# Performance work log

Measured on AMD Instinct MI355X. Metric: run time of the kernel, lower is better.

The kernel has to match this reference:

```python
import jax, jax.numpy as jnp
import numpy as np

B, S, D = 4, 2048, 768
H = 12
DH = D // H
NUM_WAY = 4
DFF = 4 * D  # FFN expansion scale=4
EPS = 1e-6


def setup_inputs() -> dict:
    key = jax.random.key(0)
    ks = jax.random.split(key, 20)
    s = 0.02
    inp = {
        "x": jax.random.normal(ks[0], (B, S, D), jnp.float32),
        "w": jax.random.randint(ks[1], (B, S), 0, NUM_WAY, jnp.int64),
        # LayerNorm 1
        "ln1_g": jnp.ones((D,), jnp.float32),
        "ln1_b": jnp.zeros((D,), jnp.float32),
        # Multi-head attention projections (input_dim=out_dim=D)
        "wq": jax.random.normal(ks[2], (D, D), jnp.float32) * s,
        "bq": jnp.zeros((D,), jnp.float32),
        "wk": jax.random.normal(ks[3], (D, D), jnp.float32) * s,
        "bk": jnp.zeros((D,), jnp.float32),
        "wv": jax.random.normal(ks[4], (D, D), jnp.float32) * s,
        "bv": jnp.zeros((D,), jnp.float32),
        "wo": jax.random.normal(ks[5], (D, D), jnp.float32) * s,
        "bo": jnp.zeros((D,), jnp.float32),
        # Way classifier
        "wcls": jax.random.normal(ks[6], (D, NUM_WAY), jnp.float32) * s,
        "bcls": jnp.zeros((NUM_WAY,), jnp.float32),
        # num_way stacked FFN experts: Linear(D,4D) -> ReLU -> Linear(4D,D)
        "w1": jax.random.normal(ks[7], (NUM_WAY, D, DFF), jnp.float32) * s,
        "b1": jnp.zeros((NUM_WAY, DFF), jnp.float32),
        "w2": jax.random.normal(ks[8], (NUM_WAY, DFF, D), jnp.float32) * s,
        "b2": jnp.zeros((NUM_WAY, D), jnp.float32),
    }
    return inp


def _layernorm(x, g, b):
    mu = jnp.mean(x, axis=-1, keepdims=True)
    var = jnp.mean(jnp.square(x - mu), axis=-1, keepdims=True)
    return (x - mu) * jax.lax.rsqrt(var + EPS) * g + b


def reference(x, w, ln1_g, ln1_b, wq, bq, wk, bk, wv, bv, wo, bo,
              wcls, bcls, w1, b1, w2, b2):
    # pre-LN
    xn = _layernorm(x, ln1_g, ln1_b)
    # multi-head self-attention (q = k = v = xn)
    q = (xn @ wq + bq).reshape(B, S, H, DH)
    k = (xn @ wk + bk).reshape(B, S, H, DH)
    v = (xn @ wv + bv).reshape(B, S, H, DH)
    scores = jnp.einsum('bqhd,bkhd->bhqk', q, k) / jnp.sqrt(jnp.float32(DH))
    attn = jax.nn.softmax(scores, axis=-1)
    ctx = jnp.einsum('bhqk,bkhd->bqhd', attn, v).reshape(B, S, D)
    ctx = ctx @ wo + bo
    # dropout is identity at inference; residual
    out = ctx + x
    # dense compute-all-experts FFN, then per-token select by routing id w
    # (mask-overwrite in original == one-hot select since masks partition)
    ffn_out = jnp.zeros_like(out)
    for ci in range(NUM_WAY):
        h = jax.nn.relu(out @ w1[ci] + b1[ci])        # [B,S,4D]
        fi = h @ w2[ci] + b2[ci]                      # [B,S,D]
        mask = (w == ci).astype(out.dtype)[..., None]  # [B,S,1]
        if ci == 0:
            # original initializes ffn_out with way-0 output everywhere;
            # later ways overwrite where w == ci, net = select expert w
            ffn_out = fi
        else:
            ffn_out = ffn_out * (1.0 - mask) + fi * mask
    way_logits = out @ wcls + bcls  # [B,S,NUM_WAY]
    return ffn_out, way_logits
```

## Files before the change

kernel.cpp:

```cpp
#include <hip/hip_runtime.h>
#include <cstdint>

typedef unsigned short u16;
typedef float f32x4 __attribute__((ext_vector_type(4)));
typedef float f32x16 __attribute__((ext_vector_type(16)));
typedef __bf16 bf16x8 __attribute__((ext_vector_type(8)));

#define LOG2E 1.44269504088896340736f

__device__ __forceinline__ u16 f2bf(float f) {
    union { float f; unsigned u; } v; v.f = f;
    unsigned r = v.u + 0x7fffu + ((v.u >> 16) & 1u);
    return (u16)(r >> 16);
}

__device__ __forceinline__ unsigned cvt_pk_bf16(float lo, float hi) {
    unsigned r;
    asm("v_cvt_pk_bf16_f32 %0, %1, %2" : "=v"(r) : "v"(lo), "v"(hi));
    return r;
}

__device__ __forceinline__ float exp2_hw(float x) {
    float r;
    asm("v_exp_f32 %0, %1" : "=v"(r) : "v"(x));
    return r;
}

__device__ __forceinline__ f32x4 mfma16(bf16x8 a, bf16x8 b, f32x4 c) {
    return __builtin_amdgcn_mfma_f32_16x16x32_bf16(a, b, c, 0, 0, 0);
}

__device__ __forceinline__ f32x16 mfma32(bf16x8 a, bf16x8 b, f32x16 c) {
    return __builtin_amdgcn_mfma_f32_32x32x16_bf16(a, b, c, 0, 0, 0);
}

__device__ __forceinline__ void gload_lds16(const void* g, void* l) {
    __builtin_amdgcn_global_load_lds(
        (__attribute__((address_space(1))) unsigned int*)(g),
        (__attribute__((address_space(3))) unsigned int*)(l),
        16, 0, 0);
}

#define MB_TOK 8192
#define DM 768
#define HH 12
#define DHD 64
#define NWAY 4
#define DFF 3072
#define SEQ 2048
#define NBATCH 4

__global__ __launch_bounds__(256) void ln_kernel(
    const float* __restrict__ x, const float* __restrict__ g,
    const float* __restrict__ bb, u16* __restrict__ xn)
{
    int row = blockIdx.x, t = threadIdx.x;
    const float* xr = x + (size_t)row * DM;
    float v0 = xr[t], v1 = xr[t + 256], v2 = xr[t + 512];
    float s = v0 + v1 + v2;
    __shared__ float red[4];
    #pragma unroll
    for (int k = 1; k < 64; k <<= 1) s += __shfl_xor(s, k);
    if ((t & 63) == 0) red[t >> 6] = s;
    __syncthreads();
    float mu = (red[0] + red[1] + red[2] + red[3]) * (1.f / 768.f);
    float d0 = v0 - mu, d1 = v1 - mu, d2 = v2 - mu;
    float q = d0 * d0 + d1 * d1 + d2 * d2;
    #pragma unroll
    for (int k = 1; k < 64; k <<= 1) q += __shfl_xor(q, k);
    __syncthreads();
    if ((t & 63) == 0) red[t >> 6] = q;
    __syncthreads();
    float var = (red[0] + red[1] + red[2] + red[3]) * (1.f / 768.f);
    float rs = rsqrtf(var + 1e-6f);
    u16* xo = xn + (size_t)row * DM;
    xo[t]       = f2bf(d0 * rs * g[t]       + bb[t]);
    xo[t + 256] = f2bf(d1 * rs * g[t + 256] + bb[t + 256]);
    xo[t + 512] = f2bf(d2 * rs * g[t + 512] + bb[t + 512]);
}

__global__ __launch_bounds__(256) void transpose_bf16(
    const float* __restrict__ src, u16* __restrict__ dst, int K, int N)
{
    __shared__ float tl[32][33];
    size_t bofs = (size_t)blockIdx.z * K * N;
    src += bofs; dst += bofs;
    int n0 = blockIdx.x * 32, k0 = blockIdx.y * 32;
    int tx = threadIdx.x, ty = threadIdx.y;
    #pragma unroll
    for (int j = 0; j < 4; ++j)
        tl[ty + j * 8][tx] = src[(size_t)(k0 + ty + j * 8) * N + n0 + tx];
    __syncthreads();
    #pragma unroll
    for (int j = 0; j < 4; ++j)
        dst[(size_t)(n0 + ty + j * 8) * K + k0 + tx] = f2bf(tl[tx][ty + j * 8]);
}

__global__ __launch_bounds__(256) void vT_kernel(
    const u16* __restrict__ qkv, u16* __restrict__ vT)
{
    __shared__ u16 tl[32][33];
    int bh = blockIdx.z;
    int b = bh / HH, h = bh % HH;
    int key0 = blockIdx.x * 32;
    int d0 = blockIdx.y * 32;
    int tx = threadIdx.x, ty = threadIdx.y;
    const u16* src = qkv + ((size_t)b * SEQ + key0) * 2304 + 1536 + h * 64 + d0;
    #pragma unroll
    for (int j = 0; j < 4; ++j)
        tl[ty + j * 8][tx] = src[(size_t)(ty + j * 8) * 2304 + tx];
    __syncthreads();
    u16* dst = vT + ((size_t)bh * 64 + d0) * SEQ + key0;
    #pragma unroll
    for (int j = 0; j < 4; ++j)
        dst[(size_t)(ty + j * 8) * SEQ + tx] = tl[tx][ty + j * 8];
}

__global__ void concat_bias_kernel(const float* bq, const float* bk,
                                   const float* bv, float* bqkv)
{
    int i = blockIdx.x * 256 + threadIdx.x;
    if (i < 2304) bqkv[i] = i < 768 ? bq[i] : (i < 1536 ? bk[i - 768] : bv[i - 1536]);
}

__global__ void route_kernel(const int* __restrict__ wl,
                             int* __restrict__ perm, int* __restrict__ eoff,
                             int4* __restrict__ fmap)
{
    __shared__ int cnt[4], cur[4], off[5];
    int tid = threadIdx.x;
    if (tid < 4) cnt[tid] = 0;
    __syncthreads();
    for (int t = tid; t < MB_TOK; t += 256) atomicAdd(&cnt[wl[t] & 3], 1);
    __syncthreads();
    if (tid == 0) {
        off[0] = 0;
        for (int e = 0; e < 4; ++e) off[e + 1] = off[e] + cnt[e];
        int idx = 0;
        for (int e = 0; e < 4; ++e)
            for (int s = 0; s < cnt[e]; s += 128)
                fmap[idx++] = make_int4(e, off[e], s, cnt[e] - s);
        for (; idx < 68; ++idx) fmap[idx] = make_int4(-1, 0, 0, 0);
        for (int e = 0; e < 5; ++e) eoff[e] = off[e];
        for (int e = 0; e < 4; ++e) cur[e] = off[e];
    }
    __syncthreads();
    for (int t = tid; t < MB_TOK; t += 256) {
        int e = wl[t] & 3;
        int pos = atomicAdd(&cur[e], 1);
        perm[pos] = t;
    }
}

template<int MODE, bool RELU, bool RES, bool ST32, bool ST16>
__global__ __launch_bounds__(256, 2) void gemm_bt_kernel(
    const u16* __restrict__ A, const u16* __restrict__ Bt,
    const float* __restrict__ bias, const float* __restrict__ res,
    float* __restrict__ out32, u16* __restrict__ out16,
    int M, int N, int K, int ntn,
    const int* __restrict__ perm, const int4* __restrict__ fmap)
{
    __shared__ __attribute__((aligned(16))) u16 As[128 * 32];
    __shared__ __attribute__((aligned(16))) u16 Bs[128 * 32];
    int tid = threadIdx.x;
    int wv = tid >> 6, ln = tid & 63;
    int bt = blockIdx.x / ntn;
    int tn = (blockIdx.x % ntn) * 128;

    int seg = 0, ms = 0, mb = 128, tm = 0;
    if (MODE != 0) {
        int4 ent = fmap[bt];
        if (ent.x < 0) return;
        seg = ent.y; ms = ent.z; mb = ent.w; if (mb > 128) mb = 128;
        Bt += (size_t)ent.x * N * K;
        bias += ent.x * N;
    } else {
        tm = bt * 128;
    }

    f32x4 acc[4][4];
    #pragma unroll
    for (int i = 0; i < 4; ++i)
        #pragma unroll
        for (int j = 0; j < 4; ++j) acc[i][j] = f32x4{0.f, 0.f, 0.f, 0.f};

    int wr = wv >> 1, wc = wv & 1;
    int lr = ln & 15, hi = ln >> 4;
    int nk = K / 32;

    for (int kk = 0; kk < nk; ++kk) {
        int k0 = kk * 32;
        #pragma unroll
        for (int i = 0; i < 2; ++i) {
            int r = (wv * 2 + i) * 16 + (ln >> 2);
            int am = r < mb ? r : (mb - 1);
            size_t arow;
            if (MODE == 1)      arow = (size_t)perm[seg + ms + am];
            else if (MODE == 2) arow = (size_t)(seg + ms + am);
            else                arow = (size_t)(tm + r);
            gload_lds16(A + arow * K + k0 + (ln & 3) * 8, &As[(wv * 2 + i) * 512]);
        }
        #pragma unroll
        for (int i = 0; i < 2; ++i) {
            int r = (wv * 2 + i) * 16 + (ln >> 2);
            gload_lds16(Bt + (size_t)(tn + r) * K + k0 + (ln & 3) * 8,
                        &Bs[(wv * 2 + i) * 512]);
        }
        __syncthreads();
        bf16x8 a[4], b[4];
        #pragma unroll
        for (int m = 0; m < 4; ++m)
            a[m] = *(const bf16x8*)&As[(wr * 64 + m * 16 + lr) * 32 + hi * 8];
        #pragma unroll
        for (int n = 0; n < 4; ++n)
            b[n] = *(const bf16x8*)&Bs[(wc * 64 + n * 16 + lr) * 32 + hi * 8];
        #pragma unroll
        for (int m = 0; m < 4; ++m)
            #pragma unroll
            for (int n = 0; n < 4; ++n)
                acc[m][n] = mfma16(a[m], b[n], acc[m][n]);
        __syncthreads();
    }

    #pragma unroll
    for (int m = 0; m < 4; ++m) {
        int rb = wr * 64 + m * 16 + hi * 4;
        #pragma unroll
        for (int n = 0; n < 4; ++n) {
            int gcol = tn + wc * 64 + n * 16 + lr;
            float bvv = bias[gcol];
            #pragma unroll
            for (int i = 0; i < 4; ++i) {
                int rml = rb + i;
                float v = acc[m][n][i] + bvv;
                if (RELU) v = v > 0.f ? v : 0.f;
                if (MODE == 0) {
                    size_t grow = (size_t)(tm + rml);
                    if (RES) v += res[grow * N + gcol];
                    if (ST32) out32[grow * N + gcol] = v;
                    if (ST16) out16[grow * N + gcol] = f2bf(v);
                } else {
                    if (rml < mb) {
                        size_t orow = (MODE == 1) ? (size_t)(seg + ms + rml)
                                                  : (size_t)perm[seg + ms + rml];
                        if (ST32) out32[orow * N + gcol] = v;
                        if (ST16) out16[orow * N + gcol] = f2bf(v);
                    }
                }
            }
        }
    }
}

__global__ __launch_bounds__(256, 4) void attn_kernel(
    const u16* __restrict__ qkv, const u16* __restrict__ vT,
    u16* __restrict__ ctx)
{
    __shared__ __attribute__((aligned(16))) u16 Ks[2][4096];
    __shared__ __attribute__((aligned(16))) u16 Vs[2][4096];
    int tid = threadIdx.x;
    int wv = tid >> 6, ln = tid & 63;
    int qv = ln & 31, hi = ln >> 5;
    int bid = blockIdx.x;
    int bh = (bid & 7) * 6 + ((bid >> 3) % 6);
    int qt = (bid >> 3) / 6;
    int b = bh / HH, h = bh % HH;
    int q0 = qt * 128 + wv * 32;
    size_t qrowb = (size_t)(b * SEQ + q0);
    const float C = 0.125f * LOG2E;

    bf16x8 qf[4];
    {
        const u16* qp = qkv + (qrowb + qv) * 2304 + h * 64 + hi * 8;
        #pragma unroll
        for (int ds = 0; ds < 4; ++ds) qf[ds] = *(const bf16x8*)(qp + ds * 16);
    }

    int csrc = 8 * ((ln & 7) ^ (ln >> 3));
    const size_t kbase = (size_t)b * SEQ * 2304 + 768 + h * 64;
    const u16* vtb = vT + (size_t)bh * 64 * SEQ;
    const u16* kp0 = qkv + kbase + (size_t)(wv * 16 + (ln >> 3)) * 2304 + csrc;
    const u16* kp1 = kp0 + (size_t)8 * 2304;
    const u16* vp0 = vtb + (size_t)(wv * 16 + (ln >> 3)) * SEQ + csrc;
    const u16* vp1 = vp0 + (size_t)8 * SEQ;

#define ATTN_STAGE(bf_, t_) do {                                          \
    gload_lds16(kp0 + (size_t)(t_) * 64 * 2304, &Ks[bf_][(wv * 2) * 512]);\
    gload_lds16(kp1 + (size_t)(t_) * 64 * 2304, &Ks[bf_][(wv * 2 + 1) * 512]);\
    gload_lds16(vp0 + (size_t)(t_) * 64, &Vs[bf_][(wv * 2) * 512]);       \
    gload_lds16(vp1 + (size_t)(t_) * 64, &Vs[bf_][(wv * 2 + 1) * 512]);   \
} while (0)

    f32x16 oacc[2];
    #pragma unroll
    for (int i = 0; i < 2; ++i)
        #pragma unroll
        for (int r = 0; r < 16; ++r) oacc[i][r] = 0.f;
    float m_run = -INFINITY, l_run = 0.f;
    int ksw = (qv & 7) * 8;

    ATTN_STAGE(0, 0);

    for (int kt = 0; kt < SEQ / 64; ++kt) {
        int bf = kt & 1;
        __syncthreads();
        if (kt + 1 < SEQ / 64) ATTN_STAGE(bf ^ 1, kt + 1);

        f32x16 s0, s1;
        #pragma unroll
        for (int r = 0; r < 16; ++r) { s0[r] = 0.f; s1[r] = 0.f; }
        #pragma unroll
        for (int ds = 0; ds < 4; ++ds) {
            bf16x8 ka0 = *(const bf16x8*)&Ks[bf][qv * 64 + ((ds * 16 + hi * 8) ^ ksw)];
            bf16x8 ka1 = *(const bf16x8*)&Ks[bf][(32 + qv) * 64 + ((ds * 16 + hi * 8) ^ ksw)];
            s0 = mfma32(ka0, qf[ds], s0);
            s1 = mfma32(ka1, qf[ds], s1);
        }

        float tmax = s0[0];
        #pragma unroll
        for (int r = 1; r < 16; ++r) tmax = fmaxf(tmax, s0[r]);
        #pragma unroll
        for (int r = 0; r < 16; ++r) tmax = fmaxf(tmax, s1[r]);
        tmax = fmaxf(tmax, __shfl_xor(tmax, 32));

        if (!__all(tmax - m_run <= 64.f)) {
            float m_new = fmaxf(m_run, tmax);
            float corr = exp2_hw((m_run - m_new) * C);
            l_run *= corr;
            #pragma unroll
            for (int i = 0; i < 2; ++i)
                #pragma unroll
                for (int r = 0; r < 16; ++r) oacc[i][r] *= corr;
            m_run = m_new;
        }
        float c2 = -m_run * C;
        float psum = 0.f;
        #pragma unroll
        for (int r = 0; r < 16; ++r) {
            s0[r] = exp2_hw(fmaf(s0[r], C, c2)); psum += s0[r];
            s1[r] = exp2_hw(fmaf(s1[r], C, c2)); psum += s1[r];
        }
        l_run += psum;

        #pragma unroll
        for (int kb = 0; kb < 2; ++kb) {
            #pragma unroll
            for (int hc = 0; hc < 2; ++hc) {
                const f32x16& sv = kb ? s1 : s0;
                unsigned x0 = cvt_pk_bf16(sv[8 * hc + 0], sv[8 * hc + 1]);
                unsigned x1 = cvt_pk_bf16(sv[8 * hc + 2], sv[8 * hc + 3]);
                unsigned x2 = cvt_pk_bf16(sv[8 * hc + 4], sv[8 * hc + 5]);
                unsigned x3 = cvt_pk_bf16(sv[8 * hc + 6], sv[8 * hc + 7]);
                unsigned t0 = hi ? x0 : x2, t1 = hi ? x1 : x3;
                unsigned r0 = (unsigned)__shfl_xor((int)t0, 32);
                unsigned r1 = (unsigned)__shfl_xor((int)t1, 32);
                union { bf16x8 v; unsigned u[4]; } pf;
                pf.u[0] = hi ? r0 : x0; pf.u[1] = hi ? r1 : x1;
                pf.u[2] = hi ? x2 : r0; pf.u[3] = hi ? x3 : r1;
                int kc = (kb * 32 + hc * 16 + hi * 8) ^ ksw;
                #pragma unroll
                for (int dblk = 0; dblk < 2; ++dblk) {
                    bf16x8 va = *(const bf16x8*)&Vs[bf][(dblk * 32 + qv) * 64 + kc];
                    oacc[dblk] = mfma32(va, pf.v, oacc[dblk]);
                }
            }
        }
    }
#undef ATTN_STAGE

    float l_tot = l_run + __shfl_xor(l_run, 32);
    float inv = 1.f / l_tot;

    __syncthreads();
    u16* eb = &Ks[0][0] + wv * 2048;
    #pragma unroll
    for (int dblk = 0; dblk < 2; ++dblk)
        #pragma unroll
        for (int r = 0; r < 16; r += 2) {
            int d = dblk * 32 + (r & 3) + 8 * (r >> 2) + 4 * hi;
            unsigned pk = cvt_pk_bf16(oacc[dblk][r] * inv, oacc[dblk][r + 1] * inv);
            *(unsigned*)&eb[qv * 64 + (d ^ ((qv & 7) * 8))] = pk;
        }
    __syncthreads();
    {
        u16* ctr = ctx + (qrowb + qv) * DM + h * 64 + hi * 32;
        #pragma unroll
        for (int g = 0; g < 4; ++g) {
            bf16x8 vv = *(const bf16x8*)&eb[qv * 64 + ((hi * 32 + g * 8) ^ ((qv & 7) * 8))];
            *(bf16x8*)(ctr + g * 8) = vv;
        }
    }
}

__global__ __launch_bounds__(256) void cls_kernel(
    const float* __restrict__ outm, const float* __restrict__ wcls,
    const float* __restrict__ bcls, float* __restrict__ dst)
{
    int row = blockIdx.x, t = threadIdx.x;
    const float* xr = outm + (size_t)row * DM;
    float a0 = 0, a1 = 0, a2 = 0, a3 = 0;
    for (int j = t; j < DM; j += 256) {
        float xv = xr[j];
        float4 wv4 = *(const float4*)(const void*)(wcls + (size_t)j * 4);
        a0 += xv * wv4.x; a1 += xv * wv4.y; a2 += xv * wv4.z; a3 += xv * wv4.w;
    }
    #pragma unroll
    for (int k = 1; k < 64; k <<= 1) {
        a0 += __shfl_xor(a0, k); a1 += __shfl_xor(a1, k);
        a2 += __shfl_xor(a2, k); a3 += __shfl_xor(a3, k);
    }
    __shared__ float red[4][4];
    if ((t & 63) == 0) {
        int wid = t >> 6;
        red[wid][0] = a0; red[wid][1] = a1; red[wid][2] = a2; red[wid][3] = a3;
    }
    __syncthreads();
    if (t < 4)
        dst[(size_t)row * 4 + t] =
            red[0][t] + red[1][t] + red[2][t] + red[3][t] + bcls[t];
}

extern "C" void kernel_launch(void* const* d_in, const int* in_sizes, int n_in,
                              void* d_out, int out_size, void* d_ws, size_t ws_size,
                              hipStream_t stream) {
    const float* x      = (const float*)d_in[0];
    const int*   wl     = (const int*)d_in[1];
    const float* ln_g   = (const float*)d_in[2];
    const float* ln_b   = (const float*)d_in[3];
    const float* wq     = (const float*)d_in[4];
    const float* bq     = (const float*)d_in[5];
    const float* wk     = (const float*)d_in[6];
    const float* bk     = (const float*)d_in[7];
    const float* wvv    = (const float*)d_in[8];
    const float* bv     = (const float*)d_in[9];
    const float* wo     = (const float*)d_in[10];
    const float* bo     = (const float*)d_in[11];
    const float* wcls   = (const float*)d_in[12];
    const float* bcls   = (const float*)d_in[13];
    const float* w1     = (const float*)d_in[14];
    const float* b1     = (const float*)d_in[15];
    const float* w2     = (const float*)d_in[16];
    const float* b2     = (const float*)d_in[17];
    float* out = (float*)d_out;

    char* ws = (char*)d_ws;
    u16*   xn    = (u16*)  (ws + 0);
    u16*   qkv   = (u16*)  (ws + 12582912);
    u16*   hbuf  = (u16*)  (ws + 0);
    u16*   ctx   = (u16*)  (ws + 50331648);
    u16*   outb  = (u16*)  (ws + 62914560);
    u16*   wqkvt = (u16*)  (ws + 75497472);
    u16*   wot   = (u16*)  (ws + 79036416);
    u16*   w1t   = (u16*)  (ws + 80216064);
    u16*   w2t   = (u16*)  (ws + 99090432);
    float* bqkv  = (float*)(ws + 117964800);
    int*   perm  = (int*)  (ws + 117974016);
    int*   eoff  = (int*)  (ws + 118006784);
    int4*  fmap  = (int4*) (ws + 118006816);
    u16*   vT    = (u16*)  (ws + 118008064);
    float* outf  = out;

    route_kernel<<<1, 256, 0, stream>>>(wl, perm, eoff, fmap);
    concat_bias_kernel<<<9, 256, 0, stream>>>(bq, bk, bv, bqkv);
    dim3 tb(32, 8);
    transpose_bf16<<<dim3(24, 24, 1), tb, 0, stream>>>(wq,  wqkvt,             768, 768);
    transpose_bf16<<<dim3(24, 24, 1), tb, 0, stream>>>(wk,  wqkvt + 768 * 768, 768, 768);
    transpose_bf16<<<dim3(24, 24, 1), tb, 0, stream>>>(wvv, wqkvt + 2 * 768 * 768, 768, 768);
    transpose_bf16<<<dim3(24, 24, 1), tb, 0, stream>>>(wo,  wot, 768, 768);
    transpose_bf16<<<dim3(96, 24, 4), tb, 0, stream>>>(w1,  w1t, 768, 3072);
    transpose_bf16<<<dim3(24, 96, 4), tb, 0, stream>>>(w2,  w2t, 3072, 768);
    ln_kernel<<<MB_TOK, 256, 0, stream>>>(x, ln_g, ln_b, xn);

    gemm_bt_kernel<0, false, false, false, true><<<64 * 18, 256, 0, stream>>>(
        xn, wqkvt, bqkv, nullptr, nullptr, qkv, MB_TOK, 2304, 768, 18, nullptr, nullptr);

    vT_kernel<<<dim3(64, 2, 48), tb, 0, stream>>>(qkv, vT);

    attn_kernel<<<768, 256, 0, stream>>>(qkv, vT, ctx);

    gemm_bt_kernel<0, false, true, true, true><<<64 * 6, 256, 0, stream>>>(
        ctx, wot, bo, x, outf, outb, MB_TOK, 768, 768, 6, nullptr, nullptr);

    cls_kernel<<<MB_TOK, 256, 0, stream>>>(outf, wcls, bcls, out + (size_t)MB_TOK * DM);

    gemm_bt_kernel<1, true, false, false, true><<<68 * 24, 256, 0, stream>>>(
        outb, w1t, b1, nullptr, nullptr, hbuf, MB_TOK, DFF, 768, 24, perm, fmap);

    gemm_bt_kernel<2, false, false, true, false><<<68 * 6, 256, 0, stream>>>(
        hbuf, w2t, b2, nullptr, out, nullptr, MB_TOK, 768, DFF, 6, perm, fmap);
}
```

Before: 376.5 us.

## Double-buffer GEMM LDS tiles and swizzle block order across XCDs

```diff
diff --git a/kernel.cpp b/kernel.cpp
--- a/kernel.cpp
+++ b/kernel.cpp
@@ -140,7 +140,7 @@
         for (int e = 0; e < 4; ++e)
             for (int s = 0; s < cnt[e]; s += 128)
                 fmap[idx++] = make_int4(e, off[e], s, cnt[e] - s);
-        for (; idx < 68; ++idx) fmap[idx] = make_int4(-1, 0, 0, 0);
+        for (; idx < 72; ++idx) fmap[idx] = make_int4(-1, 0, 0, 0);
         for (int e = 0; e < 5; ++e) eoff[e] = off[e];
         for (int e = 0; e < 4; ++e) cur[e] = off[e];
     }
@@ -153,19 +153,22 @@
 }
 
 template<int MODE, bool RELU, bool RES, bool ST32, bool ST16>
-__global__ __launch_bounds__(256, 2) void gemm_bt_kernel(
+__global__ __launch_bounds__(256, 3) void gemm_bt_kernel(
     const u16* __restrict__ A, const u16* __restrict__ Bt,
     const float* __restrict__ bias, const float* __restrict__ res,
     float* __restrict__ out32, u16* __restrict__ out16,
-    int M, int N, int K, int ntn,
+    int nbt, int N, int K, int ntn,
     const int* __restrict__ perm, const int4* __restrict__ fmap)
 {
-    __shared__ __attribute__((aligned(16))) u16 As[128 * 32];
-    __shared__ __attribute__((aligned(16))) u16 Bs[128 * 32];
+    __shared__ __attribute__((aligned(16))) u16 As[2][4096];
+    __shared__ __attribute__((aligned(16))) u16 Bs[2][4096];
     int tid = threadIdx.x;
     int wv = tid >> 6, ln = tid & 63;
-    int bt = blockIdx.x / ntn;
-    int tn = (blockIdx.x % ntn) * 128;
+    int bpx = gridDim.x / (ntn << 3);
+    int jj = blockIdx.x >> 3;
+    int bt = (blockIdx.x & 7) * bpx + jj / ntn;
+    int tn = (jj % ntn) * 128;
+    if (bt >= nbt) return;
 
     int seg = 0, ms = 0, mb = 128, tm = 0;
     if (MODE != 0) {
@@ -188,39 +191,46 @@
     int lr = ln & 15, hi = ln >> 4;
     int nk = K / 32;
 
+    const u16* asrc[2];
+    const u16* bsrc[2];
+    #pragma unroll
+    for (int i = 0; i < 2; ++i) {
+        int r = (wv * 2 + i) * 16 + (ln >> 2);
+        int am = r < mb ? r : (mb - 1);
+        size_t arow;
+        if (MODE == 1)      arow = (size_t)perm[seg + ms + am];
+        else if (MODE == 2) arow = (size_t)(seg + ms + am);
+        else                arow = (size_t)(tm + r);
+        asrc[i] = A + arow * K + (ln & 3) * 8;
+        bsrc[i] = Bt + (size_t)(tn + r) * K + (ln & 3) * 8;
+    }
+
+#define GSTAGE(bf_, k0_) do {                                             \
+    gload_lds16(asrc[0] + (k0_), &As[bf_][(wv * 2) * 512]);               \
+    gload_lds16(asrc[1] + (k0_), &As[bf_][(wv * 2 + 1) * 512]);           \
+    gload_lds16(bsrc[0] + (k0_), &Bs[bf_][(wv * 2) * 512]);               \
+    gload_lds16(bsrc[1] + (k0_), &Bs[bf_][(wv * 2 + 1) * 512]);           \
+} while (0)
+
+    GSTAGE(0, 0);
     for (int kk = 0; kk < nk; ++kk) {
-        int k0 = kk * 32;
-        #pragma unroll
-        for (int i = 0; i < 2; ++i) {
-            int r = (wv * 2 + i) * 16 + (ln >> 2);
-            int am = r < mb ? r : (mb - 1);
-            size_t arow;
-            if (MODE == 1)      arow = (size_t)perm[seg + ms + am];
-            else if (MODE == 2) arow = (size_t)(seg + ms + am);
-            else                arow = (size_t)(tm + r);
-            gload_lds16(A + arow * K + k0 + (ln & 3) * 8, &As[(wv * 2 + i) * 512]);
-        }
-        #pragma unroll
-        for (int i = 0; i < 2; ++i) {
-            int r = (wv * 2 + i) * 16 + (ln >> 2);
-            gload_lds16(Bt + (size_t)(tn + r) * K + k0 + (ln & 3) * 8,
-                        &Bs[(wv * 2 + i) * 512]);
-        }
+        int bf = kk & 1;
         __syncthreads();
+        if (kk + 1 < nk) GSTAGE(bf ^ 1, (kk + 1) * 32);
         bf16x8 a[4], b[4];
         #pragma unroll
         for (int m = 0; m < 4; ++m)
-            a[m] = *(const bf16x8*)&As[(wr * 64 + m * 16 + lr) * 32 + hi * 8];
+            a[m] = *(const bf16x8*)&As[bf][(wr * 64 + m * 16 + lr) * 32 + hi * 8];
         #pragma unroll
         for (int n = 0; n < 4; ++n)
-            b[n] = *(const bf16x8*)&Bs[(wc * 64 + n * 16 + lr) * 32 + hi * 8];
+            b[n] = *(const bf16x8*)&Bs[bf][(wc * 64 + n * 16 + lr) * 32 + hi * 8];
         #pragma unroll
         for (int m = 0; m < 4; ++m)
             #pragma unroll
             for (int n = 0; n < 4; ++n)
                 acc[m][n] = mfma16(a[m], b[n], acc[m][n]);
-        __syncthreads();
-    }
+    }
+#undef GSTAGE
 
     #pragma unroll
     for (int m = 0; m < 4; ++m) {
@@ -458,7 +468,7 @@
     int*   perm  = (int*)  (ws + 117974016);
     int*   eoff  = (int*)  (ws + 118006784);
     int4*  fmap  = (int4*) (ws + 118006816);
-    u16*   vT    = (u16*)  (ws + 118008064);
+    u16*   vT    = (u16*)  (ws + 118007968);
     float* outf  = out;
 
     route_kernel<<<1, 256, 0, stream>>>(wl, perm, eoff, fmap);
@@ -472,21 +482,21 @@
     transpose_bf16<<<dim3(24, 96, 4), tb, 0, stream>>>(w2,  w2t, 3072, 768);
     ln_kernel<<<MB_TOK, 256, 0, stream>>>(x, ln_g, ln_b, xn);
 
-    gemm_bt_kernel<0, false, false, false, true><<<64 * 18, 256, 0, stream>>>(
-        xn, wqkvt, bqkv, nullptr, nullptr, qkv, MB_TOK, 2304, 768, 18, nullptr, nullptr);
+    gemm_bt_kernel<0, false, false, false, true><<<1152, 256, 0, stream>>>(
+        xn, wqkvt, bqkv, nullptr, nullptr, qkv, 64, 2304, 768, 18, nullptr, nullptr);
 
     vT_kernel<<<dim3(64, 2, 48), tb, 0, stream>>>(qkv, vT);
 
     attn_kernel<<<768, 256, 0, stream>>>(qkv, vT, ctx);
 
-    gemm_bt_kernel<0, false, true, true, true><<<64 * 6, 256, 0, stream>>>(
-        ctx, wot, bo, x, outf, outb, MB_TOK, 768, 768, 6, nullptr, nullptr);
+    gemm_bt_kernel<0, false, true, true, true><<<384, 256, 0, stream>>>(
+        ctx, wot, bo, x, outf, outb, 64, 768, 768, 6, nullptr, nullptr);
 
     cls_kernel<<<MB_TOK, 256, 0, stream>>>(outf, wcls, bcls, out + (size_t)MB_TOK * DM);
 
-    gemm_bt_kernel<1, true, false, false, true><<<68 * 24, 256, 0, stream>>>(
-        outb, w1t, b1, nullptr, nullptr, hbuf, MB_TOK, DFF, 768, 24, perm, fmap);
-
-    gemm_bt_kernel<2, false, false, true, false><<<68 * 6, 256, 0, stream>>>(
-        hbuf, w2t, b2, nullptr, out, nullptr, MB_TOK, 768, DFF, 6, perm, fmap);
-}
+    gemm_bt_kernel<1, true, false, false, true><<<1728, 256, 0, stream>>>(
+        outb, w1t, b1, nullptr, nullptr, hbuf, 72, DFF, 768, 24, perm, fmap);
+
+    gemm_bt_kernel<2, false, false, true, false><<<432, 256, 0, stream>>>(
+        hbuf, w2t, b2, nullptr, out, nullptr, 72, 768, DFF, 6, perm, fmap);
+}
```

New measurement: 373.1 us. About the same (-0.9%).
